# Kernel optimization log

Measured on AMD Instinct MI355X. Metric: run time of the kernel, lower is better.

## Reference

```python
import jax, jax.numpy as jnp
import numpy as np


def _fake_quant(x, scale, qmin, qmax):
    # per-tensor int8 fake quant: scale -> round -> clamp -> dequant
    q = jnp.clip(jnp.round(x / scale), qmin, qmax)
    return q * scale


def setup_inputs() -> dict:
    key = jax.random.key(0)
    k1, k2, k3 = jax.random.split(key, 3)
    B, IN, OUT = 4096, 2048, 8192
    x = jax.random.normal(k1, (B, IN), dtype=jnp.float32)
    weight = jax.random.normal(k2, (OUT, IN), dtype=jnp.float32) * 0.02
    bias = jax.random.normal(k3, (OUT,), dtype=jnp.float32) * 0.01
    mul_val = jnp.full((1,), 200.0, dtype=jnp.float32)
    return {"x": x, "weight": weight, "bias": bias, "mul_val": mul_val}


def reference(x, weight, bias, mul_val):
    # Int8ActPerTensorFloat: signed, non-narrow range [-128, 127]
    act_scale = jnp.max(jnp.abs(x)) / 128.0
    xq = _fake_quant(x, act_scale, -128.0, 127.0)
    # Int8WeightPerTensorFloat: signed, narrow range [-127, 127]
    w_scale = jnp.max(jnp.abs(weight)) / 127.0
    wq = _fake_quant(weight, w_scale, -127.0, 127.0)
    # linear: y = xq @ wq.T + b, then elementwise scalar multiply
    y = jnp.einsum("bi,oi->bo", xq, wq) + bias
    return mul_val * y
```

## Files before the change

### kernel.cpp

```cpp
#include <hip/hip_runtime.h>


typedef int v4i  __attribute__((ext_vector_type(4)));
typedef int v16i __attribute__((ext_vector_type(16)));

#define MDIM 4096
#define NDIM 8192
#define KDIM 2048
#define NT   (KDIM / 64)

typedef __attribute__((address_space(1))) void* gas_ptr;
typedef __attribute__((address_space(3))) void* las_ptr;

#define XBLK 1024

__global__ __launch_bounds__(256) void absmax2(const float4* __restrict__ x,
                                               const float4* __restrict__ w,
                                               float* __restrict__ partial) {
    const int tid = threadIdx.x;
    const bool isx = blockIdx.x < XBLK;
    float m0 = 0.0f, m1 = 0.0f;
    if (isx) {
        const size_t base = (size_t)blockIdx.x * 256 + tid;
#pragma unroll
        for (int j = 0; j < 8; j += 2) {
            float4 v0 = x[base + (size_t)j * 262144];
            float4 v1 = x[base + (size_t)(j + 1) * 262144];
            m0 = fmaxf(m0, fmaxf(fmaxf(fabsf(v0.x), fabsf(v0.y)),
                                 fmaxf(fabsf(v0.z), fabsf(v0.w))));
            m1 = fmaxf(m1, fmaxf(fmaxf(fabsf(v1.x), fabsf(v1.y)),
                                 fmaxf(fabsf(v1.z), fabsf(v1.w))));
        }
    } else {
        const size_t base = (size_t)(blockIdx.x - XBLK) * 256 + tid;
#pragma unroll
        for (int j = 0; j < 8; j += 2) {
            float4 v0 = w[base + (size_t)j * 524288];
            float4 v1 = w[base + (size_t)(j + 1) * 524288];
            m0 = fmaxf(m0, fmaxf(fmaxf(fabsf(v0.x), fabsf(v0.y)),
                                 fmaxf(fabsf(v0.z), fabsf(v0.w))));
            m1 = fmaxf(m1, fmaxf(fmaxf(fabsf(v1.x), fabsf(v1.y)),
                                 fmaxf(fabsf(v1.z), fabsf(v1.w))));
        }
    }
    float m = fmaxf(m0, m1);
#pragma unroll
    for (int off = 32; off > 0; off >>= 1)
        m = fmaxf(m, __shfl_xor(m, off, 64));
    __shared__ float wm[4];
    if ((tid & 63) == 0) wm[tid >> 6] = m;
    __syncthreads();
    if (tid == 0)
        partial[blockIdx.x] = fmaxf(fmaxf(wm[0], wm[1]), fmaxf(wm[2], wm[3]));
}

__global__ __launch_bounds__(256) void quant2(const float4* __restrict__ x,
                                              v4i* __restrict__ qxp,
                                              const float4* __restrict__ w,
                                              v4i* __restrict__ qwp,
                                              const float* __restrict__ partial,
                                              unsigned* __restrict__ scales) {
    const int tid = threadIdx.x;
    float gx = 0.0f, gw = 0.0f;
#pragma unroll
    for (int j = 0; j < 4; ++j) gx = fmaxf(gx, partial[tid + j * 256]);
#pragma unroll
    for (int j = 0; j < 8; ++j) gw = fmaxf(gw, partial[XBLK + tid + j * 256]);
#pragma unroll
    for (int off = 32; off > 0; off >>= 1) {
        gx = fmaxf(gx, __shfl_xor(gx, off, 64));
        gw = fmaxf(gw, __shfl_xor(gw, off, 64));
    }
    __shared__ float smx[4], smw[4];
    if ((tid & 63) == 0) { smx[tid >> 6] = gx; smw[tid >> 6] = gw; }
    __syncthreads();
    const float fmx = fmaxf(fmaxf(smx[0], smx[1]), fmaxf(smx[2], smx[3]));
    const float fmw = fmaxf(fmaxf(smw[0], smw[1]), fmaxf(smw[2], smw[3]));
    if (blockIdx.x == 0 && tid == 0) {
        scales[0] = __float_as_uint(fmx);
        scales[1] = __float_as_uint(fmw);
    }
    const float sxs = fmx / 128.0f;
    const float sws = fmw / 127.0f;

    const bool isx = blockIdx.x < XBLK;
    const float4* in = isx ? x : w;
    v4i* outp = isx ? qxp : qwp;
    const int total = isx ? (MDIM * KDIM / 16) : (NDIM * KDIM / 16);
    const int nb = isx ? XBLK : (3072 - XBLK);
    const int b  = isx ? blockIdx.x : (blockIdx.x - XBLK);
    const float s  = isx ? sxs : sws;
    const float lo = isx ? -128.0f : -127.0f;
    for (int idx = b * 256 + tid; idx < total; idx += nb * 256) {
        const int c   = idx & 3;
        const int r   = (idx >> 2) & 255;
        const int kt  = (idx >> 10) & 31;
        const int blk = idx >> 15;
        const float4* src = in + (size_t)(blk * 256 + r) * (KDIM / 4) + kt * 16 + c * 4;
        int q[4];
#pragma unroll
        for (int j = 0; j < 4; ++j) {
            float4 v = src[j];
            int b0 = (int)fminf(fmaxf(rintf(v.x / s), lo), 127.0f);
            int b1 = (int)fminf(fmaxf(rintf(v.y / s), lo), 127.0f);
            int b2 = (int)fminf(fmaxf(rintf(v.z / s), lo), 127.0f);
            int b3 = (int)fminf(fmaxf(rintf(v.w / s), lo), 127.0f);
            q[j] = (b0 & 255) | ((b1 & 255) << 8) | ((b2 & 255) << 16) | (b3 << 24);
        }
        v4i qq; qq[0] = q[0]; qq[1] = q[1]; qq[2] = q[2]; qq[3] = q[3];
        outp[((size_t)(blk * 32 + kt) * 4 + c) * 256 + r] = qq;
    }
}

__global__ __launch_bounds__(512, 2) void gemm_i8(
    const signed char* __restrict__ qxp, const signed char* __restrict__ qwp,
    const float* __restrict__ bias, const float* __restrict__ mulv,
    const unsigned* __restrict__ scales, float* __restrict__ out) {
    __shared__ signed char ldsA[4][16384];
    __shared__ signed char ldsB[4][16384];

    const int t    = threadIdx.x;
    const int lane = t & 63;
    const int ln   = lane & 31;
    const int hi   = lane >> 5;
    const int w    = t >> 6;
    const int wr   = w >> 2;
    const int wc   = w & 3;

    const int orig = blockIdx.x;
    const int wg   = ((orig & 7) << 6) | (orig >> 3);
    const int bm   = wg >> 5;
    const int bn   = wg & 31;

    const signed char* srcA = qxp + (size_t)bm * (32 * 16384);
    const signed char* srcB = qwp + (size_t)bn * (32 * 16384);
    signed char* dA = &ldsA[0][0] + t * 16;
    signed char* dB = &ldsB[0][0] + t * 16;

    auto stage = [&](int buf, int kt) {
        const signed char* sa = srcA + kt * 16384 + t * 16;
        const signed char* sb = srcB + kt * 16384 + t * 16;
        __builtin_amdgcn_global_load_lds((gas_ptr)sa,          (las_ptr)(dA + buf * 16384),        16, 0, 0);
        __builtin_amdgcn_global_load_lds((gas_ptr)(sa + 8192), (las_ptr)(dA + buf * 16384 + 8192), 16, 0, 0);
        __builtin_amdgcn_global_load_lds((gas_ptr)sb,          (las_ptr)(dB + buf * 16384),        16, 0, 0);
        __builtin_amdgcn_global_load_lds((gas_ptr)(sb + 8192), (las_ptr)(dB + buf * 16384 + 8192), 16, 0, 0);
    };

    const int aOff = (wr * 128 + ln) * 16;
    const int bOff = (wc * 64  + ln) * 16;

    v16i acc[4][2];
#pragma unroll
    for (int mt = 0; mt < 4; ++mt)
#pragma unroll
        for (int nt = 0; nt < 2; ++nt)
#pragma unroll
            for (int r = 0; r < 16; ++r) acc[mt][nt][r] = 0;

    auto phase = [&](int kt, int stageKt) {
        const int buf = kt & 3;
        const signed char* A0 = &ldsA[buf][0] + hi * 4096;
        const signed char* B0 = &ldsB[buf][0] + hi * 4096;
        const signed char* A1 = &ldsA[buf][0] + (2 + hi) * 4096;
        const signed char* B1 = &ldsB[buf][0] + (2 + hi) * 4096;

        v4i a0[4], a1[4], b0[2], b1[2];
#pragma unroll
        for (int mt = 0; mt < 4; ++mt) a0[mt] = *(const v4i*)(A0 + aOff + mt * 512);
#pragma unroll
        for (int nt = 0; nt < 2; ++nt) b0[nt] = *(const v4i*)(B0 + bOff + nt * 512);
#pragma unroll
        for (int mt = 0; mt < 4; ++mt) a1[mt] = *(const v4i*)(A1 + aOff + mt * 512);
#pragma unroll
        for (int nt = 0; nt < 2; ++nt) b1[nt] = *(const v4i*)(B1 + bOff + nt * 512);

        if (stageKt < NT) stage(stageKt & 3, stageKt);
        __builtin_amdgcn_s_barrier();
        __builtin_amdgcn_s_setprio(1);
#pragma unroll
        for (int mt = 0; mt < 4; ++mt)
#pragma unroll
            for (int nt = 0; nt < 2; ++nt)
                acc[mt][nt] = __builtin_amdgcn_mfma_i32_32x32x32_i8(
                    a0[mt], b0[nt], acc[mt][nt], 0, 0, 0);
#pragma unroll
        for (int mt = 0; mt < 4; ++mt)
#pragma unroll
            for (int nt = 0; nt < 2; ++nt)
                acc[mt][nt] = __builtin_amdgcn_mfma_i32_32x32x32_i8(
                    a1[mt], b1[nt], acc[mt][nt], 0, 0, 0);
        __builtin_amdgcn_s_setprio(0);
    };

    stage(0, 0);
    stage(1, 1);
    stage(2, 2);
    asm volatile("s_waitcnt vmcnt(4)" ::: "memory");
    __builtin_amdgcn_s_barrier();

    for (int j = 0; j < 15; ++j) {
        phase(2 * j, 2 * j + 3);
        __builtin_amdgcn_s_barrier();
        phase(2 * j + 1, 2 * j + 4);
        asm volatile("s_waitcnt vmcnt(4)" ::: "memory");
        __builtin_amdgcn_s_barrier();
    }
    phase(30, NT);
    asm volatile("s_waitcnt vmcnt(0)" ::: "memory");
    __builtin_amdgcn_s_barrier();
    phase(31, NT);

    const float fm = mulv[0];
    const float fs = fm * (__uint_as_float(scales[0]) / 128.0f)
                        * (__uint_as_float(scales[1]) / 127.0f);
    const int colb = bn * 256 + wc * 64 + ln;
    const int hi4  = hi * 4;
#pragma unroll
    for (int nt = 0; nt < 2; ++nt) {
        const int ocol = colb + nt * 32;
        const float bv = bias[ocol] * fm;
#pragma unroll
        for (int mt = 0; mt < 4; ++mt) {
            float* op = out + (size_t)(bm * 256 + wr * 128 + mt * 32) * NDIM + ocol;
#pragma unroll
            for (int r = 0; r < 16; ++r) {
                const int row = (r & 3) + 8 * (r >> 2) + hi4;
                op[(size_t)row * NDIM] = fs * (float)acc[mt][nt][r] + bv;
            }
        }
    }
}

extern "C" void kernel_launch(void* const* d_in, const int* in_sizes, int n_in,
                              void* d_out, int out_size, void* d_ws, size_t ws_size,
                              hipStream_t stream) {
    const float4* x    = (const float4*)d_in[0];
    const float4* wgt  = (const float4*)d_in[1];
    const float*  bias = (const float*)d_in[2];
    const float*  mulv = (const float*)d_in[3];
    float* out = (float*)d_out;

    unsigned* scales  = (unsigned*)d_ws;
    float*    partial = (float*)((char*)d_ws + 256);
    signed char* qxp  = (signed char*)d_ws + 256 + 16384;
    signed char* qwp  = qxp + (size_t)MDIM * KDIM;

    absmax2<<<3072, 256, 0, stream>>>(x, wgt, partial);
    quant2<<<3072, 256, 0, stream>>>(x, (v4i*)qxp, wgt, (v4i*)qwp,
                                     partial, scales);
    gemm_i8<<<512, 512, 0, stream>>>(qxp, qwp, bias, mulv, scales, out);
}
```

Measured before the change: 125.6 us.

## Split each K-tile into four interleaved sub-phases of LDS reads, loads and MFMAs

Restructures the GEMM main loop so that each K-tile runs as four sub-phases. Each sub-phase issues one global-to-LDS load, reads a small set of LDS fragments, and runs four MFMAs, with barriers and lgkmcnt waits placed between sub-phases. This is a finer-grained ping-pong schedule meant to overlap LDS reads and global loads with matrix-core work and to lower register pressure. The cost is many more barriers per tile and vmcnt accounting that now counts individual loads, which is easy to get wrong.

After: 130.5 us. 3.9% more time.

```diff
diff --git a/kernel.cpp b/kernel.cpp
--- a/kernel.cpp
+++ b/kernel.cpp
@@ -137,18 +137,37 @@
     signed char* dA = &ldsA[0][0] + t * 16;
     signed char* dB = &ldsB[0][0] + t * 16;
 
-    auto stage = [&](int buf, int kt) {
-        const signed char* sa = srcA + kt * 16384 + t * 16;
-        const signed char* sb = srcB + kt * 16384 + t * 16;
-        __builtin_amdgcn_global_load_lds((gas_ptr)sa,          (las_ptr)(dA + buf * 16384),        16, 0, 0);
-        __builtin_amdgcn_global_load_lds((gas_ptr)(sa + 8192), (las_ptr)(dA + buf * 16384 + 8192), 16, 0, 0);
-        __builtin_amdgcn_global_load_lds((gas_ptr)sb,          (las_ptr)(dB + buf * 16384),        16, 0, 0);
-        __builtin_amdgcn_global_load_lds((gas_ptr)(sb + 8192), (las_ptr)(dB + buf * 16384 + 8192), 16, 0, 0);
+    auto stage1 = [&](int kt, int part) {
+        if (kt >= NT) return;
+        const int buf = kt & 3;
+        if (part == 0)
+            __builtin_amdgcn_global_load_lds((gas_ptr)(srcA + kt * 16384 + t * 16),
+                                             (las_ptr)(dA + buf * 16384), 16, 0, 0);
+        else if (part == 1)
+            __builtin_amdgcn_global_load_lds((gas_ptr)(srcA + kt * 16384 + 8192 + t * 16),
+                                             (las_ptr)(dA + buf * 16384 + 8192), 16, 0, 0);
+        else if (part == 2)
+            __builtin_amdgcn_global_load_lds((gas_ptr)(srcB + kt * 16384 + t * 16),
+                                             (las_ptr)(dB + buf * 16384), 16, 0, 0);
+        else
+            __builtin_amdgcn_global_load_lds((gas_ptr)(srcB + kt * 16384 + 8192 + t * 16),
+                                             (las_ptr)(dB + buf * 16384 + 8192), 16, 0, 0);
+    };
+
+    auto waitv = [&](int n) {
+        if (n == 8)      asm volatile("s_waitcnt vmcnt(8)" ::: "memory");
+        else if (n == 4) asm volatile("s_waitcnt vmcnt(4)" ::: "memory");
+        else if (n == 0) asm volatile("s_waitcnt vmcnt(0)" ::: "memory");
     };
 
     const int aOff = (wr * 128 + ln) * 16;
     const int bOff = (wc * 64  + ln) * 16;
 
+#define RD(base, plane, off) (*(const v4i*)((base) + (plane) * 4096 + (off)))
+#define MF(A, B, C) __builtin_amdgcn_mfma_i32_32x32x32_i8(A, B, C, 0, 0, 0)
+#define LGKM0 do { asm volatile("s_waitcnt lgkmcnt(0)" ::: "memory"); \
+                   __builtin_amdgcn_sched_barrier(0); } while (0)
+
     v16i acc[4][2];
 #pragma unroll
     for (int mt = 0; mt < 4; ++mt)
@@ -157,58 +176,76 @@
 #pragma unroll
             for (int r = 0; r < 16; ++r) acc[mt][nt][r] = 0;
 
-    auto phase = [&](int kt, int stageKt) {
-        const int buf = kt & 3;
-        const signed char* A0 = &ldsA[buf][0] + hi * 4096;
-        const signed char* B0 = &ldsB[buf][0] + hi * 4096;
-        const signed char* A1 = &ldsA[buf][0] + (2 + hi) * 4096;
-        const signed char* B1 = &ldsB[buf][0] + (2 + hi) * 4096;
-
-        v4i a0[4], a1[4], b0[2], b1[2];
-#pragma unroll
-        for (int mt = 0; mt < 4; ++mt) a0[mt] = *(const v4i*)(A0 + aOff + mt * 512);
-#pragma unroll
-        for (int nt = 0; nt < 2; ++nt) b0[nt] = *(const v4i*)(B0 + bOff + nt * 512);
-#pragma unroll
-        for (int mt = 0; mt < 4; ++mt) a1[mt] = *(const v4i*)(A1 + aOff + mt * 512);
-#pragma unroll
-        for (int nt = 0; nt < 2; ++nt) b1[nt] = *(const v4i*)(B1 + bOff + nt * 512);
-
-        if (stageKt < NT) stage(stageKt & 3, stageKt);
-        __builtin_amdgcn_s_barrier();
-        __builtin_amdgcn_s_setprio(1);
-#pragma unroll
-        for (int mt = 0; mt < 4; ++mt)
-#pragma unroll
-            for (int nt = 0; nt < 2; ++nt)
-                acc[mt][nt] = __builtin_amdgcn_mfma_i32_32x32x32_i8(
-                    a0[mt], b0[nt], acc[mt][nt], 0, 0, 0);
-#pragma unroll
-        for (int mt = 0; mt < 4; ++mt)
-#pragma unroll
-            for (int nt = 0; nt < 2; ++nt)
-                acc[mt][nt] = __builtin_amdgcn_mfma_i32_32x32x32_i8(
-                    a1[mt], b1[nt], acc[mt][nt], 0, 0, 0);
-        __builtin_amdgcn_s_setprio(0);
+    auto tile4 = [&](int buf, int sT, int wn) {
+        const signed char* Ab = &ldsA[buf][0];
+        const signed char* Bb = &ldsB[buf][0];
+        v4i aA0, aA1, aA2, aA3;
+        v4i aB0, aB1, aB2, aB3;
+        v4i b00, b01, b10, b11;
+
+        aA0 = RD(Ab, hi, aOff);          aA1 = RD(Ab, hi, aOff + 512);
+        aA2 = RD(Ab, 2 + hi, aOff);      aA3 = RD(Ab, 2 + hi, aOff + 512);
+        b00 = RD(Bb, hi, bOff);          b01 = RD(Bb, 2 + hi, bOff);
+        stage1(sT, 0);
+        __builtin_amdgcn_s_barrier();
+        LGKM0;
+        __builtin_amdgcn_s_setprio(1);
+        acc[0][0] = MF(aA0, b00, acc[0][0]);
+        acc[0][0] = MF(aA2, b01, acc[0][0]);
+        acc[1][0] = MF(aA1, b00, acc[1][0]);
+        acc[1][0] = MF(aA3, b01, acc[1][0]);
+        __builtin_amdgcn_s_setprio(0);
+        __builtin_amdgcn_s_barrier();
+
+        b10 = RD(Bb, hi, bOff + 512);    b11 = RD(Bb, 2 + hi, bOff + 512);
+        stage1(sT, 1);
+        __builtin_amdgcn_s_barrier();
+        LGKM0;
+        __builtin_amdgcn_s_setprio(1);
+        acc[0][1] = MF(aA0, b10, acc[0][1]);
+        acc[0][1] = MF(aA2, b11, acc[0][1]);
+        acc[1][1] = MF(aA1, b10, acc[1][1]);
+        acc[1][1] = MF(aA3, b11, acc[1][1]);
+        __builtin_amdgcn_s_setprio(0);
+        __builtin_amdgcn_s_barrier();
+
+        aB0 = RD(Ab, hi, aOff + 1024);   aB1 = RD(Ab, hi, aOff + 1536);
+        aB2 = RD(Ab, 2 + hi, aOff + 1024); aB3 = RD(Ab, 2 + hi, aOff + 1536);
+        stage1(sT, 2);
+        __builtin_amdgcn_s_barrier();
+        LGKM0;
+        __builtin_amdgcn_s_setprio(1);
+        acc[2][1] = MF(aB0, b10, acc[2][1]);
+        acc[2][1] = MF(aB2, b11, acc[2][1]);
+        acc[3][1] = MF(aB1, b10, acc[3][1]);
+        acc[3][1] = MF(aB3, b11, acc[3][1]);
+        __builtin_amdgcn_s_setprio(0);
+        __builtin_amdgcn_s_barrier();
+
+        stage1(sT, 3);
+        __builtin_amdgcn_s_barrier();
+        __builtin_amdgcn_s_setprio(1);
+        acc[2][0] = MF(aB0, b00, acc[2][0]);
+        acc[2][0] = MF(aB2, b01, acc[2][0]);
+        acc[3][0] = MF(aB1, b00, acc[3][0]);
+        acc[3][0] = MF(aB3, b01, acc[3][0]);
+        __builtin_amdgcn_s_setprio(0);
+        if (wn >= 0) waitv(wn);
+        __builtin_amdgcn_s_barrier();
     };
 
-    stage(0, 0);
-    stage(1, 1);
-    stage(2, 2);
-    asm volatile("s_waitcnt vmcnt(4)" ::: "memory");
+#pragma unroll
+    for (int kt = 0; kt < 3; ++kt)
+#pragma unroll
+        for (int p = 0; p < 4; ++p) stage1(kt, p);
+    asm volatile("s_waitcnt vmcnt(8)" ::: "memory");
     __builtin_amdgcn_s_barrier();
 
-    for (int j = 0; j < 15; ++j) {
-        phase(2 * j, 2 * j + 3);
-        __builtin_amdgcn_s_barrier();
-        phase(2 * j + 1, 2 * j + 4);
-        asm volatile("s_waitcnt vmcnt(4)" ::: "memory");
-        __builtin_amdgcn_s_barrier();
-    }
-    phase(30, NT);
-    asm volatile("s_waitcnt vmcnt(0)" ::: "memory");
-    __builtin_amdgcn_s_barrier();
-    phase(31, NT);
+    for (int j = 0; j < 16; ++j) {
+        tile4((2 * j) & 3, 2 * j + 3, (j <= 14) ? 8 : 0);
+        tile4((2 * j + 1) & 3, 2 * j + 4,
+              (j < 14) ? 8 : ((j == 14) ? 4 : -1));
+    }
 
     const float fm = mulv[0];
     const float fs = fm * (__uint_as_float(scales[0]) / 128.0f)
@@ -229,6 +266,9 @@
             }
         }
     }
+#undef RD
+#undef MF
+#undef LGKM0
 }
 
 extern "C" void kernel_launch(void* const* d_in, const int* in_sizes, int n_in,
```
